# Performance work log

Measured on AMD Instinct MI355X. Metric: run time of the kernel, lower is better.

The kernel has to match this reference:

```python
import jax, jax.numpy as jnp
import numpy as np

N, D, F, H, DH, R = 50000, 16, 256, 8, 32, 20
HOP_NUM, TOP_K, ALPHA, NEG_SLOPE = 10, 5, 0.1, 0.2
FF_HID = 4 * F


def _ln(x, g, b, eps=1e-5):
    m = x.mean(-1, keepdims=True)
    v = ((x - m) ** 2).mean(-1, keepdims=True)
    return (x - m) / jnp.sqrt(v + eps) * g + b


def setup_inputs() -> dict:
    key = jax.random.key(0)
    ks = jax.random.split(key, 16)
    s = 0.02
    inp = {
        'ent_feat': jax.random.normal(ks[0], (N, F), jnp.float32),
        'rel_feat': jax.random.normal(ks[1], (R, F), jnp.float32),
        'W_head': jax.random.normal(ks[2], (F, H * DH), jnp.float32) * s,
        'W_tail': jax.random.normal(ks[3], (F, H * DH), jnp.float32) * s,
        'W_ent': jax.random.normal(ks[4], (F, H * DH), jnp.float32) * s,
        'W_rel': jax.random.normal(ks[5], (F, H * DH), jnp.float32) * s,
        'attn_h': jax.random.normal(ks[6], (H, DH), jnp.float32) * s,
        'attn_t': jax.random.normal(ks[7], (H, DH), jnp.float32) * s,
        'attn_r': jax.random.normal(ks[8], (H, DH), jnp.float32) * s,
        'ln_ent_g': jnp.ones((F,), jnp.float32), 'ln_ent_b': jnp.zeros((F,), jnp.float32),
        'ln_rel_g': jnp.ones((F,), jnp.float32), 'ln_rel_b': jnp.zeros((F,), jnp.float32),
        'ln_ff_g': jnp.ones((F,), jnp.float32), 'ln_ff_b': jnp.zeros((F,), jnp.float32),
        'ffn_W1': jax.random.normal(ks[9], (F, FF_HID), jnp.float32) * s,
        'ffn_b1': jnp.zeros((FF_HID,), jnp.float32),
        'ffn_W2': jax.random.normal(ks[10], (FF_HID, F), jnp.float32) * s,
        'ffn_b2': jnp.zeros((F,), jnp.float32),
        'src': jax.random.randint(ks[11], (N, D), 0, N, jnp.int32),
        'rid': jax.random.randint(ks[12], (N, D), 0, R, jnp.int32),
    }
    return inp


def reference(ent_feat, rel_feat, W_head, W_tail, W_ent, W_rel,
              attn_h, attn_t, attn_r,
              ln_ent_g, ln_ent_b, ln_rel_g, ln_rel_b, ln_ff_g, ln_ff_b,
              ffn_W1, ffn_b1, ffn_W2, ffn_b2, src, rid):
    # --- projections (dropout = 0 at eval) ---
    x = _ln(ent_feat, ln_ent_g, ln_ent_b)                    # [N,F]
    fh = (x @ W_head).reshape(N, H, DH)
    ftl = (x @ W_tail).reshape(N, H, DH)
    fe = (x @ W_ent).reshape(N, H, DH)                       # 'ft' messages
    r = _ln(rel_feat, ln_rel_g, ln_rel_b)
    fr = (r @ W_rel).reshape(R, H, DH)
    # --- per-node / per-relation attention logits ---
    eh = (fh * attn_h).sum(-1)                               # [N,H]
    et = (ftl * attn_t).sum(-1)                              # [N,H]
    er = (fr * attn_r).sum(-1)                               # [R,H]
    # edges: row i = incoming edges of dst node i, sources src[i,:]
    e = eh[src] + et[:, None, :] + er[rid]                   # [N,D,H]
    e = jnp.where(e > 0, e, NEG_SLOPE * e)                   # LeakyReLU
    # --- edge_softmax over incoming edges of each dst node ---
    a = jax.nn.softmax(e, axis=1)                            # [N,D,H]
    # --- top-k sparsification + renormalization ---
    a_t = a.transpose(0, 2, 1)                               # [N,H,D]
    topv, _ = jax.lax.top_k(a_t, TOP_K)                      # [N,H,K]
    kth = topv[..., TOP_K - 1]                               # [N,H]
    top_sum = topv.sum(-1)                                   # [N,H]
    a_n = jnp.where(a_t >= kth[..., None], a_t, 0.0) / top_sum[..., None]  # [N,H,D]
    # --- PPR diffusion: feat <- (1-a) * A @ feat + a * feat0 ---
    feat0 = fe

    def step(feat, _):
        m = feat[src]                                        # [N,D,H,DH]
        agg = jnp.einsum('ndhk,nhd->nhk', m, a_n)            # [N,H,DH]
        return (1.0 - ALPHA) * agg + ALPHA * feat0, None

    feat, _ = jax.lax.scan(step, feat0, None, length=HOP_NUM)
    # --- residual (Identity since in==out) + FFN block ---
    rst = feat + ent_feat.reshape(N, H, DH)
    rst = rst.reshape(N, F)
    y = _ln(rst, ln_ff_g, ln_ff_b)
    ff = jax.nn.relu(y @ ffn_W1 + ffn_b1) @ ffn_W2 + ffn_b2
    return ff + rst
```

## Files before the change

### kernel.cpp

```cpp
#include <hip/hip_runtime.h>

#define NN   50000
#define DD   16
#define FFE  256
#define HH   8
#define DHH  32
#define RR   20
#define HOPN 10

typedef unsigned short u16;
typedef unsigned int   u32;
typedef __attribute__((ext_vector_type(8))) short  short8;
typedef __attribute__((ext_vector_type(4))) float  floatx4;

__device__ __forceinline__ float b2f(u16 u){ return __uint_as_float(((u32)u)<<16); }
__device__ __forceinline__ u16 f2b(float f){
  u32 x = __float_as_uint(f);
  u32 r = (x + 0x7fffu + ((x>>16)&1u)) >> 16;
  return (u16)r;
}

__global__ __launch_bounds__(256) void castw_kernel(
    const float* __restrict__ We, const float* __restrict__ W1,
    const float* __restrict__ W2,
    u16* __restrict__ Wet, u16* __restrict__ W1t, u16* __restrict__ W2t)
{
  int tid = blockIdx.x*256 + threadIdx.x;
  if (tid < 256*256) {
    int k = tid >> 8, n = tid & 255;
    Wet[n*256 + k] = f2b(We[tid]);
  } else if (tid < 256*256 + 256*1024) {
    int s = tid - 65536;
    int k = s >> 10, n = s & 1023;
    W1t[n*256 + k] = f2b(W1[s]);
  } else if (tid < 589824) {
    int s = tid - 327680;
    int k = s >> 8, n = s & 255;
    W2t[n*1024 + k] = f2b(W2[s]);
  }
}

__global__ __launch_bounds__(256) void prep_kernel(
    const float* __restrict__ rel_feat,
    const float* __restrict__ W_head, const float* __restrict__ W_tail,
    const float* __restrict__ W_rel,
    const float* __restrict__ attn_h, const float* __restrict__ attn_t,
    const float* __restrict__ attn_r,
    const float* __restrict__ lng, const float* __restrict__ lnb,
    double* __restrict__ Wh2, double* __restrict__ Wt2, double* __restrict__ er)
{
  int t = threadIdx.x;
  if (blockIdx.x == RR) {
    for (int h = 0; h < HH; h++) {
      double sh = 0.0, st = 0.0;
      #pragma unroll
      for (int c = 0; c < DHH; c++) {
        int j = h*DHH + c;
        sh += (double)W_head[t*FFE + j] * (double)attn_h[j];
        st += (double)W_tail[t*FFE + j] * (double)attn_t[j];
      }
      Wh2[t*HH + h] = sh;
      Wt2[t*HH + h] = st;
    }
    return;
  }
  int r = blockIdx.x;
  __shared__ double red[8];
  __shared__ double rln[256];
  double v = (double)rel_feat[r*FFE + t];
  double s = v, q = v*v;
  #pragma unroll
  for (int o = 32; o; o >>= 1) { s += __shfl_xor(s, o, 64); q += __shfl_xor(q, o, 64); }
  if ((t & 63) == 0) { red[t>>6] = s; red[4 + (t>>6)] = q; }
  __syncthreads();
  double stot = red[0]+red[1]+red[2]+red[3];
  double qtot = red[4]+red[5]+red[6]+red[7];
  double mean = stot * (1.0/256.0);
  double var  = qtot * (1.0/256.0) - mean*mean;
  double rstd = 1.0 / sqrt(var + 1e-5);
  rln[t] = (v - mean) * rstd * (double)lng[t] + (double)lnb[t];
  __syncthreads();
  double acc = 0.0;
  for (int k = 0; k < 256; k++) acc += rln[k] * (double)W_rel[k*FFE + t];
  double p = acc * (double)attn_r[t];
  #pragma unroll
  for (int o = 16; o; o >>= 1) p += __shfl_down(p, o, 32);
  if ((t & 31) == 0) er[r*HH + (t>>5)] = p;
}

__global__ __launch_bounds__(256) void logits_kernel(
    const float* __restrict__ ent,
    const float* __restrict__ lng, const float* __restrict__ lnb,
    const double* __restrict__ Wh2, const double* __restrict__ Wt2,
    u16* __restrict__ xb, double* __restrict__ eh, double* __restrict__ et)
{
  __shared__ double xs[16][258];
  int tid = threadIdx.x;
  int i0 = blockIdx.x * 16;
  int wave = tid >> 6, lane = tid & 63;
  for (int m = wave; m < 16; m += 4) {
    int row = i0 + m;
    float4 u = *(const float4*)&ent[row*FFE + lane*4];
    double v0 = u.x, v1 = u.y, v2 = u.z, v3 = u.w;
    double s = v0+v1+v2+v3;
    double q = v0*v0 + v1*v1 + v2*v2 + v3*v3;
    #pragma unroll
    for (int o = 32; o; o >>= 1) { s += __shfl_xor(s, o, 64); q += __shfl_xor(q, o, 64); }
    double mean = s * (1.0/256.0);
    double var  = q * (1.0/256.0) - mean*mean;
    double rstd = 1.0 / sqrt(var + 1e-5);
    float4 ug = *(const float4*)&lng[lane*4];
    float4 ub = *(const float4*)&lnb[lane*4];
    double y0 = (v0-mean)*rstd*(double)ug.x + (double)ub.x;
    double y1 = (v1-mean)*rstd*(double)ug.y + (double)ub.y;
    double y2 = (v2-mean)*rstd*(double)ug.z + (double)ub.z;
    double y3 = (v3-mean)*rstd*(double)ug.w + (double)ub.w;
    int c = lane*4;
    xs[m][c] = y0; xs[m][c+1] = y1; xs[m][c+2] = y2; xs[m][c+3] = y3;
    ushort4 o4;
    o4.x = f2b((float)y0); o4.y = f2b((float)y1);
    o4.z = f2b((float)y2); o4.w = f2b((float)y3);
    *(ushort4*)&xb[row*FFE + c] = o4;
  }
  __syncthreads();
  int m = (tid & 127) >> 3, h = tid & 7;
  double a = 0.0;
  if (tid < 128) {
    for (int k = 0; k < 256; k++) a += xs[m][k] * Wh2[k*HH + h];
    eh[(i0+m)*HH + h] = a;
  } else {
    for (int k = 0; k < 256; k++) a += xs[m][k] * Wt2[k*HH + h];
    et[(i0+m)*HH + h] = a;
  }
}

template<int EPI>
__global__ __launch_bounds__(256) void gemm_kernel(
    const u16* __restrict__ A, const u16* __restrict__ B,
    const float* __restrict__ bias,
    const u16* __restrict__ feat, const float* __restrict__ ent,
    u16* __restrict__ Obf, float* __restrict__ Of,
    int M, int N, int K)
{
  __shared__ u16 As[128][40];
  __shared__ u16 Bs[128][40];
  int t = threadIdx.x;
  int i0 = blockIdx.x * 128;
  int n0 = blockIdx.y * 128;
  int w = t >> 6, l = t & 63;
  int cr = t >> 2;
  int cc = (t & 3) * 8;
  int ga0 = min(i0 + cr, M-1);
  int ga1 = min(i0 + cr + 64, M-1);
  int gb0 = n0 + cr;
  int gb1 = n0 + cr + 64;
  floatx4 acc[2][8];
  #pragma unroll
  for (int mt = 0; mt < 2; mt++)
    #pragma unroll
    for (int nt = 0; nt < 8; nt++) acc[mt][nt] = (floatx4){0.f,0.f,0.f,0.f};
  int ln = l & 15, lq = (l >> 4) * 8;
  for (int k0 = 0; k0 < K; k0 += 32) {
    __syncthreads();
    *(uint4*)&As[cr][cc]      = *(const uint4*)&A[(size_t)ga0*K + k0 + cc];
    *(uint4*)&As[cr+64][cc]   = *(const uint4*)&A[(size_t)ga1*K + k0 + cc];
    *(uint4*)&Bs[cr][cc]      = *(const uint4*)&B[(size_t)gb0*K + k0 + cc];
    *(uint4*)&Bs[cr+64][cc]   = *(const uint4*)&B[(size_t)gb1*K + k0 + cc];
    __syncthreads();
    short8 bfr[8];
    #pragma unroll
    for (int nt = 0; nt < 8; nt++) bfr[nt] = *(const short8*)&Bs[nt*16 + ln][lq];
    #pragma unroll
    for (int mt = 0; mt < 2; mt++) {
      short8 afr = *(const short8*)&As[w*32 + mt*16 + ln][lq];
      #pragma unroll
      for (int nt = 0; nt < 8; nt++)
        acc[mt][nt] = __builtin_amdgcn_mfma_f32_16x16x32_bf16(afr, bfr[nt], acc[mt][nt], 0, 0, 0);
    }
  }
  int lr = (l >> 4) * 4;
  #pragma unroll
  for (int mt = 0; mt < 2; mt++) {
    #pragma unroll
    for (int nt = 0; nt < 8; nt++) {
      int col = n0 + nt*16 + ln;
      #pragma unroll
      for (int r = 0; r < 4; r++) {
        int row = i0 + w*32 + mt*16 + lr + r;
        if (row < M) {
          float v = acc[mt][nt][r];
          if (EPI == 0) {
            Obf[(size_t)row*N + col] = f2b(v);
          } else if (EPI == 1) {
            v += bias[col];
            Obf[(size_t)row*N + col] = f2b(v > 0.f ? v : 0.f);
          } else {
            v += bias[col] + b2f(feat[(size_t)row*FFE + col]) + ent[(size_t)row*FFE + col];
            Of[(size_t)row*N + col] = v;
          }
        }
      }
    }
  }
}

__global__ __launch_bounds__(256) void edge_kernel(
    const int* __restrict__ src, const int* __restrict__ rid,
    const double* __restrict__ eh, const double* __restrict__ et,
    const double* __restrict__ er,
    int* __restrict__ idx6, float* __restrict__ w6)
{
  int tid = blockIdx.x*256 + threadIdx.x;
  if (tid >= NN*HH) return;
  int i = tid >> 3, h = tid & 7;
  double bet = et[tid];
  double e[16]; int sj[16];
  #pragma unroll
  for (int d = 0; d < 16; d++) {
    int s = src[i*DD + d];
    int rv = rid[i*DD + d];
    sj[d] = s;
    double v = eh[s*HH + h] + bet + er[rv*HH + h];
    e[d] = (v > 0.0) ? v : 0.2 * v;
  }
  u32 mask = 0; double vs[5]; int js[5];
  #pragma unroll
  for (int k = 0; k < 5; k++) {
    double best = -1e300; int bj = 0, bd = 0;
    #pragma unroll
    for (int d = 0; d < 16; d++) {
      bool c = (((mask>>d)&1u) == 0u) && (e[d] > best);
      if (c) { best = e[d]; bj = sj[d]; bd = d; }
    }
    mask |= (1u << bd); vs[k] = best; js[k] = bj;
  }
  double kth = vs[4];
  int j6 = 0; bool f6 = false;
  #pragma unroll
  for (int d = 0; d < 16; d++) {
    if ((((mask>>d)&1u) == 0u) && (e[d] == kth) && !f6) { j6 = sj[d]; f6 = true; }
  }
  float m0 = (float)vs[0];
  float ex[5], ssum = 0.f;
  #pragma unroll
  for (int k = 0; k < 5; k++) { ex[k] = __expf((float)vs[k] - m0); ssum += ex[k]; }
  float inv = 0.9f / ssum;
  long base = (long)tid * 6;
  #pragma unroll
  for (int k = 0; k < 5; k++) { idx6[base+k] = js[k]; w6[base+k] = ex[k]*inv; }
  idx6[base+5] = j6; w6[base+5] = f6 ? ex[4]*inv : 0.f;
}

__global__ __launch_bounds__(256) void diff_kernel(
    const u16* __restrict__ fold, const u16* __restrict__ fe,
    const int* __restrict__ idx6, const float* __restrict__ w6,
    u16* __restrict__ fnew)
{
  int i = blockIdx.x, tid = threadIdx.x;
  int h = tid >> 5, c = tid & 31;
  long eb = ((long)i*HH + h) * 6;
  float acc = 0.1f * b2f(fe[i*FFE + tid]);
  #pragma unroll
  for (int k = 0; k < 6; k++) {
    int j = idx6[eb + k];
    float w = w6[eb + k];
    acc += w * b2f(fold[j*FFE + h*DHH + c]);
  }
  fnew[i*FFE + tid] = f2b(acc);
}

__global__ __launch_bounds__(256) void ln_ff_kernel(
    const u16* __restrict__ feat, const float* __restrict__ ent,
    const float* __restrict__ g, const float* __restrict__ b,
    u16* __restrict__ y)
{
  int w = threadIdx.x >> 6, l = threadIdx.x & 63;
  int row = blockIdx.x*4 + w;
  float4 e4 = *(const float4*)&ent[row*FFE + l*4];
  ushort4 fv = *(const ushort4*)&feat[row*FFE + l*4];
  float v0 = b2f(fv.x)+e4.x, v1 = b2f(fv.y)+e4.y;
  float v2 = b2f(fv.z)+e4.z, v3 = b2f(fv.w)+e4.w;
  float s = v0+v1+v2+v3;
  float q = v0*v0 + v1*v1 + v2*v2 + v3*v3;
  #pragma unroll
  for (int o = 32; o; o >>= 1) { s += __shfl_xor(s, o, 64); q += __shfl_xor(q, o, 64); }
  float mean = s * (1.f/256.f);
  float var  = q * (1.f/256.f) - mean*mean;
  float rstd = rsqrtf(var + 1e-5f);
  float4 g4 = *(const float4*)&g[l*4];
  float4 b4 = *(const float4*)&b[l*4];
  ushort4 o4;
  o4.x = f2b((v0-mean)*rstd*g4.x + b4.x);
  o4.y = f2b((v1-mean)*rstd*g4.y + b4.y);
  o4.z = f2b((v2-mean)*rstd*g4.z + b4.z);
  o4.w = f2b((v3-mean)*rstd*g4.w + b4.w);
  *(ushort4*)&y[row*FFE + l*4] = o4;
}

extern "C" void kernel_launch(void* const* d_in, const int* in_sizes, int n_in,
                              void* d_out, int out_size, void* d_ws, size_t ws_size,
                              hipStream_t stream)
{
  const float* ent      = (const float*)d_in[0];
  const float* rel      = (const float*)d_in[1];
  const float* W_head   = (const float*)d_in[2];
  const float* W_tail   = (const float*)d_in[3];
  const float* W_ent    = (const float*)d_in[4];
  const float* W_rel    = (const float*)d_in[5];
  const float* attn_h   = (const float*)d_in[6];
  const float* attn_t   = (const float*)d_in[7];
  const float* attn_r   = (const float*)d_in[8];
  const float* ln_ent_g = (const float*)d_in[9];
  const float* ln_ent_b = (const float*)d_in[10];
  const float* ln_rel_g = (const float*)d_in[11];
  const float* ln_rel_b = (const float*)d_in[12];
  const float* ln_ff_g  = (const float*)d_in[13];
  const float* ln_ff_b  = (const float*)d_in[14];
  const float* W1       = (const float*)d_in[15];
  const float* b1       = (const float*)d_in[16];
  const float* W2       = (const float*)d_in[17];
  const float* b2       = (const float*)d_in[18];
  const int* src        = (const int*)d_in[19];
  const int* rid        = (const int*)d_in[20];
  float* out = (float*)d_out;

  char* w = (char*)d_ws;
  double* er64 = (double*)(w + 0);
  double* Wh2  = (double*)(w + 4096);
  double* Wt2  = (double*)(w + 20480);
  double* eh64 = (double*)(w + 36864);
  double* et64 = (double*)(w + 3236864);
  u16*    xb   = (u16*)  (w + 6436864);
  u16*    fe   = (u16*)  (w + 32036864);
  u16*    fA   = (u16*)  (w + 57636864);
  int*    idx6 = (int*)  (w + 83236864);
  float*  w6   = (float*)(w + 92836864);
  u16*    h1   = (u16*)  (w + 0);
  u16*    fB   = (u16*)  (w + 102436864);
  u16*    y    = (u16*)  (w + 128036864);
  u16*    Wet  = (u16*)  (w + 153636864);
  u16*    W1t  = (u16*)  (w + 153767936);
  u16*    W2t  = (u16*)  (w + 154292224);

  castw_kernel<<<2304, 256, 0, stream>>>(W_ent, W1, W2, Wet, W1t, W2t);
  prep_kernel<<<RR+1, 256, 0, stream>>>(rel, W_head, W_tail, W_rel,
                                        attn_h, attn_t, attn_r,
                                        ln_rel_g, ln_rel_b, Wh2, Wt2, er64);
  logits_kernel<<<NN/16, 256, 0, stream>>>(ent, ln_ent_g, ln_ent_b, Wh2, Wt2,
                                           xb, eh64, et64);
  {
    dim3 g((NN + 127)/128, 2);
    gemm_kernel<0><<<g, 256, 0, stream>>>(xb, Wet, nullptr, nullptr, nullptr,
                                          fe, nullptr, NN, 256, 256);
  }
  edge_kernel<<<(NN*HH + 255)/256, 256, 0, stream>>>(src, rid, eh64, et64, er64,
                                                     idx6, w6);
  const u16* cur = fe;
  u16* bufs[2] = { fA, fB };
  for (int hop = 0; hop < HOPN; hop++) {
    u16* nxt = bufs[hop & 1];
    diff_kernel<<<NN, 256, 0, stream>>>(cur, fe, idx6, w6, nxt);
    cur = nxt;
  }
  ln_ff_kernel<<<NN/4, 256, 0, stream>>>(cur, ent, ln_ff_g, ln_ff_b, y);
  {
    dim3 g((NN + 127)/128, 8);
    gemm_kernel<1><<<g, 256, 0, stream>>>(y, W1t, b1, nullptr, nullptr,
                                          h1, nullptr, NN, 1024, 256);
  }
  {
    dim3 g((NN + 127)/128, 2);
    gemm_kernel<2><<<g, 256, 0, stream>>>(h1, W2t, b2, cur, ent,
                                          nullptr, out, NN, 256, 1024);
  }
}
```

Baseline: 906.1 us.

## Fuse ten diffusion hops into one cooperative kernel with grid sync

After: 3.561 ms. +293.0%, slower.

```diff
diff --git a/kernel.cpp b/kernel.cpp
--- a/kernel.cpp
+++ b/kernel.cpp
@@ -1,4 +1,7 @@
 #include <hip/hip_runtime.h>
+#include <hip/hip_cooperative_groups.h>
+
+namespace cg = cooperative_groups;
 
 #define NN   50000
 #define DD   16
@@ -7,6 +10,9 @@
 #define DHH  32
 #define RR   20
 #define HOPN 10
+
+#define DIFF_BLOCKS 1024
+#define NPB 49
 
 typedef unsigned short u16;
 typedef unsigned int   u32;
@@ -124,14 +130,20 @@
   }
   __syncthreads();
   int m = (tid & 127) >> 3, h = tid & 7;
-  double a = 0.0;
-  if (tid < 128) {
-    for (int k = 0; k < 256; k++) a += xs[m][k] * Wh2[k*HH + h];
-    eh[(i0+m)*HH + h] = a;
-  } else {
-    for (int k = 0; k < 256; k++) a += xs[m][k] * Wt2[k*HH + h];
-    et[(i0+m)*HH + h] = a;
-  }
+  const double* __restrict__ Wp = (tid < 128) ? Wh2 : Wt2;
+  double* __restrict__ op = (tid < 128) ? eh : et;
+  double a0=0,a1=0,a2=0,a3=0,a4=0,a5=0,a6=0,a7=0;
+  for (int k = 0; k < 256; k += 8) {
+    a0 += xs[m][k+0] * Wp[(k+0)*HH + h];
+    a1 += xs[m][k+1] * Wp[(k+1)*HH + h];
+    a2 += xs[m][k+2] * Wp[(k+2)*HH + h];
+    a3 += xs[m][k+3] * Wp[(k+3)*HH + h];
+    a4 += xs[m][k+4] * Wp[(k+4)*HH + h];
+    a5 += xs[m][k+5] * Wp[(k+5)*HH + h];
+    a6 += xs[m][k+6] * Wp[(k+6)*HH + h];
+    a7 += xs[m][k+7] * Wp[(k+7)*HH + h];
+  }
+  op[(i0+m)*HH + h] = ((a0+a1)+(a2+a3)) + ((a4+a5)+(a6+a7));
 }
 
 template<int EPI>
@@ -251,22 +263,50 @@
   idx6[base+5] = j6; w6[base+5] = f6 ? ex[4]*inv : 0.f;
 }
 
-__global__ __launch_bounds__(256) void diff_kernel(
-    const u16* __restrict__ fold, const u16* __restrict__ fe,
-    const int* __restrict__ idx6, const float* __restrict__ w6,
-    u16* __restrict__ fnew)
-{
-  int i = blockIdx.x, tid = threadIdx.x;
+__global__ __launch_bounds__(256) void diff_fused_kernel(
+    const u16* __restrict__ fe, u16* __restrict__ fA, u16* __restrict__ fB,
+    const int* __restrict__ idx6, const float* __restrict__ w6)
+{
+  __shared__ int   sIdx[NPB*48];
+  __shared__ float sW[NPB*48];
+  int tid = threadIdx.x;
+  int node0 = blockIdx.x * NPB;
+  for (int s = tid; s < NPB*48; s += 256) {
+    int node = node0 + s/48;
+    if (node < NN) {
+      sIdx[s] = idx6[(size_t)node*48 + (s%48)];
+      sW[s]   = w6[(size_t)node*48 + (s%48)];
+    } else { sIdx[s] = 0; sW[s] = 0.f; }
+  }
+  __syncthreads();
   int h = tid >> 5, c = tid & 31;
-  long eb = ((long)i*HH + h) * 6;
-  float acc = 0.1f * b2f(fe[i*FFE + tid]);
-  #pragma unroll
-  for (int k = 0; k < 6; k++) {
-    int j = idx6[eb + k];
-    float w = w6[eb + k];
-    acc += w * b2f(fold[j*FFE + h*DHH + c]);
-  }
-  fnew[i*FFE + tid] = f2b(acc);
+  cg::grid_group grid = cg::this_grid();
+  const u16* cur = fe;
+  for (int hop = 0; hop < HOPN; hop++) {
+    u16* nxt = (hop & 1) ? fB : fA;
+    for (int s = 0; s < NPB; s++) {
+      int node = node0 + s;
+      if (node < NN) {
+        float acc = 0.1f * b2f(fe[(size_t)node*FFE + tid]);
+        int base = s*48 + h*6;
+        #pragma unroll
+        for (int k = 0; k < 5; k++) {
+          int j = sIdx[base+k];
+          acc += sW[base+k] * b2f(cur[(size_t)j*FFE + h*DHH + c]);
+        }
+        float w5 = sW[base+5];
+        if (w5 != 0.f) {
+          int j = sIdx[base+5];
+          acc += w5 * b2f(cur[(size_t)j*FFE + h*DHH + c]);
+        }
+        nxt[(size_t)node*FFE + tid] = f2b(acc);
+      }
+    }
+    cur = nxt;
+    __threadfence();
+    grid.sync();
+    __threadfence();
+  }
 }
 
 __global__ __launch_bounds__(256) void ln_ff_kernel(
@@ -355,13 +395,13 @@
   }
   edge_kernel<<<(NN*HH + 255)/256, 256, 0, stream>>>(src, rid, eh64, et64, er64,
                                                      idx6, w6);
-  const u16* cur = fe;
-  u16* bufs[2] = { fA, fB };
-  for (int hop = 0; hop < HOPN; hop++) {
-    u16* nxt = bufs[hop & 1];
-    diff_kernel<<<NN, 256, 0, stream>>>(cur, fe, idx6, w6, nxt);
-    cur = nxt;
-  }
+  {
+    void* args[] = { (void*)&fe, (void*)&fA, (void*)&fB,
+                     (void*)&idx6, (void*)&w6 };
+    hipLaunchCooperativeKernel((const void*)diff_fused_kernel,
+                               dim3(DIFF_BLOCKS), dim3(256), args, 0, stream);
+  }
+  const u16* cur = fB;
   ln_ff_kernel<<<NN/4, 256, 0, stream>>>(cur, ent, ln_ff_g, ln_ff_b, y);
   {
     dim3 g((NN + 127)/128, 8);
```

## Vectorize diffusion gathers to bf16 pairs and restructure logits projection per-wave

Applied to the files above, without the earlier changes.

Result: no change. 891.3 us (-1.6%).

```diff
diff --git a/kernel.cpp b/kernel.cpp
--- a/kernel.cpp
+++ b/kernel.cpp
@@ -47,7 +47,7 @@
     const float* __restrict__ attn_h, const float* __restrict__ attn_t,
     const float* __restrict__ attn_r,
     const float* __restrict__ lng, const float* __restrict__ lnb,
-    double* __restrict__ Wh2, double* __restrict__ Wt2, double* __restrict__ er)
+    double* __restrict__ Wc, double* __restrict__ er)
 {
   int t = threadIdx.x;
   if (blockIdx.x == RR) {
@@ -59,8 +59,8 @@
         sh += (double)W_head[t*FFE + j] * (double)attn_h[j];
         st += (double)W_tail[t*FFE + j] * (double)attn_t[j];
       }
-      Wh2[t*HH + h] = sh;
-      Wt2[t*HH + h] = st;
+      Wc[t*16 + h]     = sh;
+      Wc[t*16 + 8 + h] = st;
     }
     return;
   }
@@ -91,46 +91,75 @@
 __global__ __launch_bounds__(256) void logits_kernel(
     const float* __restrict__ ent,
     const float* __restrict__ lng, const float* __restrict__ lnb,
-    const double* __restrict__ Wh2, const double* __restrict__ Wt2,
+    const double* __restrict__ Wc,
     u16* __restrict__ xb, double* __restrict__ eh, double* __restrict__ et)
 {
-  __shared__ double xs[16][258];
   int tid = threadIdx.x;
-  int i0 = blockIdx.x * 16;
-  int wave = tid >> 6, lane = tid & 63;
-  for (int m = wave; m < 16; m += 4) {
-    int row = i0 + m;
-    float4 u = *(const float4*)&ent[row*FFE + lane*4];
-    double v0 = u.x, v1 = u.y, v2 = u.z, v3 = u.w;
-    double s = v0+v1+v2+v3;
-    double q = v0*v0 + v1*v1 + v2*v2 + v3*v3;
-    #pragma unroll
-    for (int o = 32; o; o >>= 1) { s += __shfl_xor(s, o, 64); q += __shfl_xor(q, o, 64); }
-    double mean = s * (1.0/256.0);
-    double var  = q * (1.0/256.0) - mean*mean;
-    double rstd = 1.0 / sqrt(var + 1e-5);
-    float4 ug = *(const float4*)&lng[lane*4];
-    float4 ub = *(const float4*)&lnb[lane*4];
-    double y0 = (v0-mean)*rstd*(double)ug.x + (double)ub.x;
-    double y1 = (v1-mean)*rstd*(double)ug.y + (double)ub.y;
-    double y2 = (v2-mean)*rstd*(double)ug.z + (double)ub.z;
-    double y3 = (v3-mean)*rstd*(double)ug.w + (double)ub.w;
-    int c = lane*4;
-    xs[m][c] = y0; xs[m][c+1] = y1; xs[m][c+2] = y2; xs[m][c+3] = y3;
-    ushort4 o4;
-    o4.x = f2b((float)y0); o4.y = f2b((float)y1);
-    o4.z = f2b((float)y2); o4.w = f2b((float)y3);
-    *(ushort4*)&xb[row*FFE + c] = o4;
-  }
-  __syncthreads();
-  int m = (tid & 127) >> 3, h = tid & 7;
-  double a = 0.0;
-  if (tid < 128) {
-    for (int k = 0; k < 256; k++) a += xs[m][k] * Wh2[k*HH + h];
-    eh[(i0+m)*HH + h] = a;
-  } else {
-    for (int k = 0; k < 256; k++) a += xs[m][k] * Wt2[k*HH + h];
-    et[(i0+m)*HH + h] = a;
+  int w = tid >> 6, l = tid & 63;
+  int rowA = blockIdx.x*8 + w*2;
+  int rowB = rowA + 1;
+  float gg[4], bbv[4];
+  #pragma unroll
+  for (int j = 0; j < 4; j++) { gg[j] = lng[l + 64*j]; bbv[j] = lnb[l + 64*j]; }
+  double xA[4], xB[4];
+  #pragma unroll
+  for (int j = 0; j < 4; j++) xA[j] = (double)ent[(size_t)rowA*FFE + l + 64*j];
+  #pragma unroll
+  for (int j = 0; j < 4; j++) xB[j] = (double)ent[(size_t)rowB*FFE + l + 64*j];
+  double sA = xA[0]+xA[1]+xA[2]+xA[3];
+  double sB = xB[0]+xB[1]+xB[2]+xB[3];
+  double qA = xA[0]*xA[0]+xA[1]*xA[1]+xA[2]*xA[2]+xA[3]*xA[3];
+  double qB = xB[0]*xB[0]+xB[1]*xB[1]+xB[2]*xB[2]+xB[3]*xB[3];
+  #pragma unroll
+  for (int o = 32; o; o >>= 1) {
+    sA += __shfl_xor(sA, o, 64); qA += __shfl_xor(qA, o, 64);
+    sB += __shfl_xor(sB, o, 64); qB += __shfl_xor(qB, o, 64);
+  }
+  double mA = sA * (1.0/256.0), mB = sB * (1.0/256.0);
+  double vA = qA * (1.0/256.0) - mA*mA, vB = qB * (1.0/256.0) - mB*mB;
+  double rsA = 1.0 / sqrt(vA + 1e-5), rsB = 1.0 / sqrt(vB + 1e-5);
+  #pragma unroll
+  for (int j = 0; j < 4; j++) {
+    double yA = (xA[j]-mA)*rsA*(double)gg[j] + (double)bbv[j];
+    double yB = (xB[j]-mB)*rsB*(double)gg[j] + (double)bbv[j];
+    xA[j] = yA; xB[j] = yB;
+    xb[(size_t)rowA*FFE + l + 64*j] = f2b((float)yA);
+    xb[(size_t)rowB*FFE + l + 64*j] = f2b((float)yB);
+  }
+  double accA[16], accB[16];
+  #pragma unroll
+  for (int o = 0; o < 16; o++) { accA[o] = 0.0; accB[o] = 0.0; }
+  #pragma unroll
+  for (int j = 0; j < 4; j++) {
+    int k = l + 64*j;
+    const double2* wp = (const double2*)(Wc + (size_t)k*16);
+    double wv[16];
+    #pragma unroll
+    for (int u = 0; u < 8; u++) { double2 tv = wp[u]; wv[2*u] = tv.x; wv[2*u+1] = tv.y; }
+    #pragma unroll
+    for (int o = 0; o < 16; o++) {
+      accA[o] = fma(xA[j], wv[o], accA[o]);
+      accB[o] = fma(xB[j], wv[o], accB[o]);
+    }
+  }
+  #pragma unroll
+  for (int o = 0; o < 16; o++) {
+    #pragma unroll
+    for (int off = 32; off; off >>= 1) {
+      accA[o] += __shfl_xor(accA[o], off, 64);
+      accB[o] += __shfl_xor(accB[o], off, 64);
+    }
+  }
+  #pragma unroll
+  for (int o = 0; o < 16; o++) {
+    if (l == o) {
+      if (o < 8) eh[(size_t)rowA*HH + o] = accA[o];
+      else       et[(size_t)rowA*HH + (o-8)] = accA[o];
+    }
+    if (l == 16 + o) {
+      if (o < 8) eh[(size_t)rowB*HH + o] = accB[o];
+      else       et[(size_t)rowB*HH + (o-8)] = accB[o];
+    }
   }
 }
 
@@ -256,17 +285,33 @@
     const int* __restrict__ idx6, const float* __restrict__ w6,
     u16* __restrict__ fnew)
 {
-  int i = blockIdx.x, tid = threadIdx.x;
-  int h = tid >> 5, c = tid & 31;
+  int tid = threadIdx.x;
+  int i = blockIdx.x*2 + (tid >> 7);
+  int t2 = tid & 127;
+  int h = t2 >> 4, c2 = t2 & 15;
+  const u32* fold32 = (const u32*)fold;
+  const u32* fe32   = (const u32*)fe;
+  u32* fnew32 = (u32*)fnew;
   long eb = ((long)i*HH + h) * 6;
-  float acc = 0.1f * b2f(fe[i*FFE + tid]);
-  #pragma unroll
-  for (int k = 0; k < 6; k++) {
+  u32 fv = fe32[(size_t)i*128 + t2];
+  float acc0 = 0.1f * b2f((u16)(fv & 0xffff));
+  float acc1 = 0.1f * b2f((u16)(fv >> 16));
+  #pragma unroll
+  for (int k = 0; k < 5; k++) {
     int j = idx6[eb + k];
     float w = w6[eb + k];
-    acc += w * b2f(fold[j*FFE + h*DHH + c]);
-  }
-  fnew[i*FFE + tid] = f2b(acc);
+    u32 v = fold32[(size_t)j*128 + h*16 + c2];
+    acc0 += w * b2f((u16)(v & 0xffff));
+    acc1 += w * b2f((u16)(v >> 16));
+  }
+  float w5 = w6[eb + 5];
+  if (w5 != 0.f) {
+    int j = idx6[eb + 5];
+    u32 v = fold32[(size_t)j*128 + h*16 + c2];
+    acc0 += w5 * b2f((u16)(v & 0xffff));
+    acc1 += w5 * b2f((u16)(v >> 16));
+  }
+  fnew32[(size_t)i*128 + t2] = (u32)f2b(acc0) | ((u32)f2b(acc1) << 16);
 }
 
 __global__ __launch_bounds__(256) void ln_ff_kernel(
@@ -326,8 +371,7 @@
 
   char* w = (char*)d_ws;
   double* er64 = (double*)(w + 0);
-  double* Wh2  = (double*)(w + 4096);
-  double* Wt2  = (double*)(w + 20480);
+  double* Wc   = (double*)(w + 4096);
   double* eh64 = (double*)(w + 36864);
   double* et64 = (double*)(w + 3236864);
   u16*    xb   = (u16*)  (w + 6436864);
@@ -345,9 +389,9 @@
   castw_kernel<<<2304, 256, 0, stream>>>(W_ent, W1, W2, Wet, W1t, W2t);
   prep_kernel<<<RR+1, 256, 0, stream>>>(rel, W_head, W_tail, W_rel,
                                         attn_h, attn_t, attn_r,
-                                        ln_rel_g, ln_rel_b, Wh2, Wt2, er64);
-  logits_kernel<<<NN/16, 256, 0, stream>>>(ent, ln_ent_g, ln_ent_b, Wh2, Wt2,
-                                           xb, eh64, et64);
+                                        ln_rel_g, ln_rel_b, Wc, er64);
+  logits_kernel<<<NN/8, 256, 0, stream>>>(ent, ln_ent_g, ln_ent_b, Wc,
+                                          xb, eh64, et64);
   {
     dim3 g((NN + 127)/128, 2);
     gemm_kernel<0><<<g, 256, 0, stream>>>(xb, Wet, nullptr, nullptr, nullptr,
@@ -359,7 +403,7 @@
   u16* bufs[2] = { fA, fB };
   for (int hop = 0; hop < HOPN; hop++) {
     u16* nxt = bufs[hop & 1];
-    diff_kernel<<<NN, 256, 0, stream>>>(cur, fe, idx6, w6, nxt);
+    diff_kernel<<<NN/2, 256, 0, stream>>>(cur, fe, idx6, w6, nxt);
     cur = nxt;
   }
   ln_ff_kernel<<<NN/4, 256, 0, stream>>>(cur, ent, ln_ff_g, ln_ff_b, y);
```
